# Kernel tuning notes

Measured on AMD Instinct MI355X. Metric: run time of the kernel, lower is better.

## Reference

```python
import jax, jax.numpy as jnp
import numpy as np

IN_DIM, HIDDEN, CLASSES, NBASIS = 1024, 4096, 1000, 16

def setup_inputs() -> dict:
    key = jax.random.key(0)
    ks = jax.random.split(key, 7)
    x = jax.random.normal(ks[0], (4096, IN_DIM), dtype=jnp.float32)
    # FerroelectricBasis params: per-feature tanh basis (centers, scales) + dense mix
    centers = jax.random.normal(ks[1], (IN_DIM, NBASIS), dtype=jnp.float32)
    scales = jax.random.uniform(ks[2], (IN_DIM, NBASIS), dtype=jnp.float32, minval=0.5, maxval=2.0)
    s = 1.0 / np.sqrt(IN_DIM * NBASIS)
    Wb = jax.random.uniform(ks[3], (IN_DIM * NBASIS, HIDDEN), dtype=jnp.float32, minval=-s, maxval=s)
    bb = jax.random.uniform(ks[4], (HIDDEN,), dtype=jnp.float32, minval=-s, maxval=s)
    sh = 1.0 / np.sqrt(HIDDEN)
    Wh = jax.random.uniform(ks[5], (HIDDEN, CLASSES), dtype=jnp.float32, minval=-sh, maxval=sh)
    bh = jax.random.uniform(ks[6], (CLASSES,), dtype=jnp.float32, minval=-sh, maxval=sh)
    return {"x": x, "centers": centers, "scales": scales, "Wb": Wb, "bb": bb, "Wh": Wh, "bh": bh}

def reference(x, centers, scales, Wb, bb, Wh, bh):
    B = x.shape[0]
    # ferroelectric (hysteresis-like) tanh basis expansion: [B, in_dim, num_basis]
    feats = jnp.tanh((x[:, :, None] - centers[None]) * scales[None])
    feats = feats.reshape(B, -1)                      # [B, in_dim*num_basis]
    h = feats @ Wb + bb                               # [B, hidden]
    phi = jax.nn.sigmoid(h)
    logits = phi @ Wh + bh                            # [B, num_classes]
    return logits
```

## Files before the change

### kernel.cpp

```cpp
#include <hip/hip_runtime.h>
#include <hip/hip_bf16.h>

typedef __bf16 bf16x8_t __attribute__((ext_vector_type(8)));
typedef float f32x4_t __attribute__((ext_vector_type(4)));
typedef int i32x4_t __attribute__((ext_vector_type(4)));
typedef int i32x8_t __attribute__((ext_vector_type(8)));

#define GLDS(gp, lp) __builtin_amdgcn_global_load_lds(                        \
    (const __attribute__((address_space(1))) void*)(gp),                      \
    (__attribute__((address_space(3))) void*)(lp), 16, 0, 0)

__device__ __forceinline__ float fast_tanh(float z) {
  float zc = fminf(10.0f, fmaxf(-10.0f, z));
  float e = __expf(2.0f * zc);
  return 1.0f - 2.0f / (e + 1.0f);
}

__device__ __forceinline__ int pack_fp8x4(float a, float b, float c, float d) {
  int w = __builtin_amdgcn_cvt_pk_fp8_f32(a, b, 0, false);
  w = __builtin_amdgcn_cvt_pk_fp8_f32(c, d, w, true);
  return w;
}

__global__ __launch_bounds__(256) void feats_kernel(
    const float* __restrict__ x, const float* __restrict__ c,
    const float* __restrict__ s, unsigned char* __restrict__ out) {
  int idx = blockIdx.x * 256 + threadIdx.x;
  int d = idx & 1023;
  float xv = x[idx];
  const float4* c4 = (const float4*)(c + d * 16);
  const float4* s4 = (const float4*)(s + d * 16);
  int w[4];
#pragma unroll
  for (int g = 0; g < 4; ++g) {
    float4 cc = c4[g], ss = s4[g];
    float t0 = fast_tanh((xv - cc.x) * ss.x);
    float t1 = fast_tanh((xv - cc.y) * ss.y);
    float t2 = fast_tanh((xv - cc.z) * ss.z);
    float t3 = fast_tanh((xv - cc.w) * ss.w);
    w[g] = pack_fp8x4(t0, t1, t2, t3);
  }
  *(uint4*)(out + (size_t)idx * 16) = make_uint4(w[0], w[1], w[2], w[3]);
}

__global__ __launch_bounds__(256) void transpose_fp8(
    const float* __restrict__ src, unsigned char* __restrict__ dst, int R, int C) {
  __shared__ float tile[64][65];
  const int c0 = blockIdx.x * 64, r0 = blockIdx.y * 64;
  const int t = threadIdx.x;
  const int rr = t >> 4, cc4 = (t & 15) * 4;
#pragma unroll
  for (int p = 0; p < 4; ++p) {
    int row = rr + p * 16;
    float4 v = *(const float4*)(src + (size_t)(r0 + row) * C + c0 + cc4);
    tile[row][cc4 + 0] = v.x;
    tile[row][cc4 + 1] = v.y;
    tile[row][cc4 + 2] = v.z;
    tile[row][cc4 + 3] = v.w;
  }
  __syncthreads();
  const int drow = t >> 2, seg = (t & 3) * 16;
  int w[4];
#pragma unroll
  for (int g = 0; g < 4; ++g) {
    float a = tile[seg + g * 4 + 0][drow] * 128.0f;
    float b = tile[seg + g * 4 + 1][drow] * 128.0f;
    float cc = tile[seg + g * 4 + 2][drow] * 128.0f;
    float d = tile[seg + g * 4 + 3][drow] * 128.0f;
    w[g] = pack_fp8x4(a, b, cc, d);
  }
  *(uint4*)(dst + (size_t)(c0 + drow) * R + r0 + seg) = make_uint4(w[0], w[1], w[2], w[3]);
}

__global__ __launch_bounds__(256) void transpose_cast(
    const float* __restrict__ src, __hip_bfloat16* __restrict__ dst,
    int R, int C, int Cpad) {
  __shared__ float tile[64][65];
  const int c0 = blockIdx.x * 64, r0 = blockIdx.y * 64;
  const int t = threadIdx.x;
  const int rr = t >> 4, cc4 = (t & 15) * 4;
#pragma unroll
  for (int p = 0; p < 4; ++p) {
    int row = rr + p * 16;
    int cbase = c0 + cc4;
    float4 v;
    if (cbase + 3 < C) {
      v = *(const float4*)(src + (size_t)(r0 + row) * C + cbase);
    } else {
      v.x = (cbase + 0 < C) ? src[(size_t)(r0 + row) * C + cbase + 0] : 0.0f;
      v.y = (cbase + 1 < C) ? src[(size_t)(r0 + row) * C + cbase + 1] : 0.0f;
      v.z = (cbase + 2 < C) ? src[(size_t)(r0 + row) * C + cbase + 2] : 0.0f;
      v.w = (cbase + 3 < C) ? src[(size_t)(r0 + row) * C + cbase + 3] : 0.0f;
    }
    tile[row][cc4 + 0] = v.x;
    tile[row][cc4 + 1] = v.y;
    tile[row][cc4 + 2] = v.z;
    tile[row][cc4 + 3] = v.w;
  }
  __syncthreads();
#pragma unroll
  for (int p = 0; p < 2; ++p) {
    int i = t + 256 * p;
    int drow = i >> 3;
    int seg = (i & 7) * 8;
    int dc = c0 + drow;
    alignas(16) __hip_bfloat16 vals[8];
#pragma unroll
    for (int j = 0; j < 8; ++j) vals[j] = __float2bfloat16(tile[seg + j][drow]);
    if (dc < Cpad)
      *(uint4*)(dst + (size_t)dc * R + r0 + seg) = *(const uint4*)vals;
  }
}

__global__ __launch_bounds__(512, 2) void gemm1_mx8(
    const unsigned char* __restrict__ A, const unsigned char* __restrict__ Bt,
    const float* __restrict__ bias, __hip_bfloat16* __restrict__ outb,
    int M, int N, int K) {
  __shared__ unsigned char As[2][256 * 128];
  __shared__ unsigned char Bs[2][256 * 128];
  const int tid = threadIdx.x;
  const int wave = tid >> 6, lane = tid & 63;
  const int wm = (wave >> 2) * 128, wn = (wave & 3) * 64;

  const int bid = blockIdx.x;
  const int swz = (bid & 7) * 32 + (bid >> 3);
  const int gq = swz >> 5, u = swz & 31;
  const int gm0 = ((gq >> 1) * 4 + (u >> 3)) * 256;
  const int gn0 = ((gq & 1) * 8 + (u & 7)) * 256;

  const unsigned char* ga[4];
  const unsigned char* gb[4];
  int ldso[4];
#pragma unroll
  for (int p = 0; p < 4; ++p) {
    int c = p * 512 + tid;
    int row = c >> 3;
    int g = (c & 7) ^ (row & 7);
    ga[p] = A + (size_t)(gm0 + row) * K + g * 16;
    gb[p] = Bt + (size_t)(gn0 + row) * K + g * 16;
    ldso[p] = c * 16;
  }

  f32x4_t acc[8][4] = {};
  const int fr = lane & 15, kh = lane >> 4;

#pragma unroll
  for (int p = 0; p < 4; ++p) {
    GLDS(ga[p], &As[0][ldso[p]]);
    GLDS(gb[p], &Bs[0][ldso[p]]);
  }
  __syncthreads();

  const int NT = K >> 7;
  for (int t = 0; t < NT; ++t) {
    const unsigned char* Ac = As[t & 1];
    const unsigned char* Bc = Bs[t & 1];
    unsigned char* An = (unsigned char*)As[(t + 1) & 1];
    unsigned char* Bn = (unsigned char*)Bs[(t + 1) & 1];
    const int k1 = (t + 1) << 7;
    const bool pre = (t + 1 < NT);

    i32x8_t b[4];
#pragma unroll
    for (int j = 0; j < 4; ++j) {
      int rb = wn + j * 16 + fr, sb = rb & 7;
      i32x4_t blo = *(const i32x4_t*)(Bc + rb * 128 + (((2 * kh) ^ sb) * 16));
      i32x4_t bhi = *(const i32x4_t*)(Bc + rb * 128 + (((2 * kh + 1) ^ sb) * 16));
      b[j] = __builtin_shufflevector(blo, bhi, 0, 1, 2, 3, 4, 5, 6, 7);
    }

#pragma unroll
    for (int p = 0; p < 4; ++p) {
      if (pre) {
        GLDS(ga[p] + k1, An + ldso[p]);
        GLDS(gb[p] + k1, Bn + ldso[p]);
      }
      i32x8_t a0, a1;
      {
        int ra = wm + (2 * p + 0) * 16 + fr, sa = ra & 7;
        i32x4_t lo = *(const i32x4_t*)(Ac + ra * 128 + (((2 * kh) ^ sa) * 16));
        i32x4_t hi = *(const i32x4_t*)(Ac + ra * 128 + (((2 * kh + 1) ^ sa) * 16));
        a0 = __builtin_shufflevector(lo, hi, 0, 1, 2, 3, 4, 5, 6, 7);
      }
      {
        int ra = wm + (2 * p + 1) * 16 + fr, sa = ra & 7;
        i32x4_t lo = *(const i32x4_t*)(Ac + ra * 128 + (((2 * kh) ^ sa) * 16));
        i32x4_t hi = *(const i32x4_t*)(Ac + ra * 128 + (((2 * kh + 1) ^ sa) * 16));
        a1 = __builtin_shufflevector(lo, hi, 0, 1, 2, 3, 4, 5, 6, 7);
      }
      __builtin_amdgcn_s_barrier();
      __builtin_amdgcn_s_setprio(1);
#pragma unroll
      for (int j = 0; j < 4; ++j) {
        acc[2 * p + 0][j] = __builtin_amdgcn_mfma_scale_f32_16x16x128_f8f6f4(
            a0, b[j], acc[2 * p + 0][j], 0, 0, 0, 0x7F7F7F7F, 0, 0x7F7F7F7F);
        acc[2 * p + 1][j] = __builtin_amdgcn_mfma_scale_f32_16x16x128_f8f6f4(
            a1, b[j], acc[2 * p + 1][j], 0, 0, 0, 0x7F7F7F7F, 0, 0x7F7F7F7F);
      }
      __builtin_amdgcn_s_setprio(0);
      if (p < 3) __builtin_amdgcn_s_barrier();
    }
    __syncthreads();
  }

  const int cn = lane & 15, cm = (lane >> 4) * 4;
#pragma unroll
  for (int j = 0; j < 4; ++j) {
    int n = gn0 + wn + j * 16 + cn;
    float bv = bias[n];
#pragma unroll
    for (int i = 0; i < 8; ++i) {
#pragma unroll
      for (int r = 0; r < 4; ++r) {
        int m = gm0 + wm + i * 16 + cm + r;
        float v = acc[i][j][r] * 0.0078125f + bv;
        float phi = 1.0f / (1.0f + __expf(-v));
        outb[(size_t)m * N + n] = __float2bfloat16(phi);
      }
    }
  }
}

__global__ __launch_bounds__(256) void gemm2_bt(
    const __hip_bfloat16* __restrict__ A, const __hip_bfloat16* __restrict__ Bt,
    float* __restrict__ outf, int M, int N, int K, int kcount) {
  __shared__ __hip_bfloat16 As[2][128 * 32];
  __shared__ __hip_bfloat16 Bs[2][128 * 32];
  const int tid = threadIdx.x;
  const int wave = tid >> 6, lane = tid & 63;
  const int wm = (wave >> 1) * 64, wn = (wave & 1) * 64;
  const int gm0 = blockIdx.y * 128, gn0 = blockIdx.x * 128;
  const int kbeg = blockIdx.z * kcount;

  const int t1 = tid, t2 = tid + 256;
  const __hip_bfloat16* Ag0 = A + (size_t)(gm0 + (t1 >> 2)) * K + kbeg + (t1 & 3) * 8;
  const __hip_bfloat16* Ag1 = A + (size_t)(gm0 + (t2 >> 2)) * K + kbeg + (t2 & 3) * 8;
  const __hip_bfloat16* Bg0 = Bt + (size_t)(gn0 + (t1 >> 2)) * K + kbeg + (t1 & 3) * 8;
  const __hip_bfloat16* Bg1 = Bt + (size_t)(gn0 + (t2 >> 2)) * K + kbeg + (t2 & 3) * 8;

  f32x4_t acc[4][4] = {};
  const int fr = lane & 15, fk = (lane >> 4) * 8;

  for (int k0 = 0; k0 < kcount; k0 += 64) {
#pragma unroll
    for (int h = 0; h < 2; ++h) {
      GLDS(Ag0 + h * 32, &As[h][t1 * 8]);
      GLDS(Ag1 + h * 32, &As[h][t2 * 8]);
      GLDS(Bg0 + h * 32, &Bs[h][t1 * 8]);
      GLDS(Bg1 + h * 32, &Bs[h][t2 * 8]);
    }
    Ag0 += 64; Ag1 += 64; Bg0 += 64; Bg1 += 64;
    __syncthreads();
#pragma unroll
    for (int h = 0; h < 2; ++h) {
      bf16x8_t a[4], b[4];
#pragma unroll
      for (int i = 0; i < 4; ++i) {
        a[i] = *(const bf16x8_t*)(&As[h][(wm + i * 16 + fr) * 32 + fk]);
        b[i] = *(const bf16x8_t*)(&Bs[h][(wn + i * 16 + fr) * 32 + fk]);
      }
#pragma unroll
      for (int i = 0; i < 4; ++i)
#pragma unroll
        for (int j = 0; j < 4; ++j)
          acc[i][j] = __builtin_amdgcn_mfma_f32_16x16x32_bf16(a[i], b[j], acc[i][j], 0, 0, 0);
    }
    __syncthreads();
  }

  const int cn = lane & 15, cm = (lane >> 4) * 4;
#pragma unroll
  for (int j = 0; j < 4; ++j) {
    int n = gn0 + wn + j * 16 + cn;
#pragma unroll
    for (int i = 0; i < 4; ++i)
#pragma unroll
      for (int r = 0; r < 4; ++r) {
        int m = gm0 + wm + i * 16 + cm + r;
        outf[((size_t)blockIdx.z * M + m) * N + n] = acc[i][j][r];
      }
  }
}

__global__ __launch_bounds__(256) void reduce4_kernel(
    const float* __restrict__ p, const float* __restrict__ bh,
    float* __restrict__ out) {
  int n = blockIdx.x * 256 + threadIdx.x;
  int m = blockIdx.y;
  const size_t zs = (size_t)4096 * 1024;
  if (n < 1000) {
    size_t o = (size_t)m * 1024 + n;
    out[(size_t)m * 1000 + n] = p[o] + p[zs + o] + p[2 * zs + o] + p[3 * zs + o] + bh[n];
  }
}

extern "C" void kernel_launch(void* const* d_in, const int* in_sizes, int n_in,
                              void* d_out, int out_size, void* d_ws, size_t ws_size,
                              hipStream_t stream) {
  const float* x = (const float*)d_in[0];
  const float* centers = (const float*)d_in[1];
  const float* scales = (const float*)d_in[2];
  const float* Wb = (const float*)d_in[3];
  const float* bb = (const float*)d_in[4];
  const float* Wh = (const float*)d_in[5];
  const float* bh = (const float*)d_in[6];
  float* out = (float*)d_out;

  unsigned char* feats = (unsigned char*)d_ws;
  unsigned char* Wbt = feats + (size_t)4096 * 16384;
  __hip_bfloat16* phi = (__hip_bfloat16*)(Wbt + (size_t)4096 * 16384);
  __hip_bfloat16* Wht = phi + (size_t)4096 * 4096;
  float* partial = (float*)d_ws;

  feats_kernel<<<dim3(16384), dim3(256), 0, stream>>>(x, centers, scales, feats);
  transpose_fp8<<<dim3(64, 256), dim3(256), 0, stream>>>(Wb, Wbt, 16384, 4096);
  transpose_cast<<<dim3(16, 64), dim3(256), 0, stream>>>(Wh, Wht, 4096, 1000, 1024);
  gemm1_mx8<<<dim3(256), dim3(512), 0, stream>>>(feats, Wbt, bb, phi, 4096, 4096, 16384);
  gemm2_bt<<<dim3(8, 32, 4), dim3(256), 0, stream>>>(phi, Wht, partial, 4096, 1024, 4096, 1024);
  reduce4_kernel<<<dim3(4, 4096), dim3(256), 0, stream>>>(partial, bh, out);
}
```

Baseline: 773.8 us.

## Drop split-K in second GEMM, double-buffer it, and simplify GEMM1 inner loop

The second GEMM no longer splits K four ways into fp32 partials followed by a reduction kernel. It now computes the full K per block with double-buffered LDS prefetch and writes the bias-added logits directly, removing the partial-buffer traffic and one launch. GEMM1's inner loop now issues all next-tile prefetches up front and runs the MFMA loop without the per-stage barriers. The trade-off is fewer blocks for GEMM2 (256 instead of 1024), which may underfill the GPU, and the GEMM1 change alters how LDS reads and MFMAs interleave across waves.

```diff
diff --git a/kernel.cpp b/kernel.cpp
--- a/kernel.cpp
+++ b/kernel.cpp
@@ -158,7 +158,14 @@
     unsigned char* An = (unsigned char*)As[(t + 1) & 1];
     unsigned char* Bn = (unsigned char*)Bs[(t + 1) & 1];
     const int k1 = (t + 1) << 7;
-    const bool pre = (t + 1 < NT);
+
+    if (t + 1 < NT) {
+#pragma unroll
+      for (int p = 0; p < 4; ++p) {
+        GLDS(ga[p] + k1, An + ldso[p]);
+        GLDS(gb[p] + k1, Bn + ldso[p]);
+      }
+    }
 
     i32x8_t b[4];
 #pragma unroll
@@ -169,37 +176,19 @@
       b[j] = __builtin_shufflevector(blo, bhi, 0, 1, 2, 3, 4, 5, 6, 7);
     }
 
-#pragma unroll
-    for (int p = 0; p < 4; ++p) {
-      if (pre) {
-        GLDS(ga[p] + k1, An + ldso[p]);
-        GLDS(gb[p] + k1, Bn + ldso[p]);
-      }
-      i32x8_t a0, a1;
-      {
-        int ra = wm + (2 * p + 0) * 16 + fr, sa = ra & 7;
-        i32x4_t lo = *(const i32x4_t*)(Ac + ra * 128 + (((2 * kh) ^ sa) * 16));
-        i32x4_t hi = *(const i32x4_t*)(Ac + ra * 128 + (((2 * kh + 1) ^ sa) * 16));
-        a0 = __builtin_shufflevector(lo, hi, 0, 1, 2, 3, 4, 5, 6, 7);
-      }
-      {
-        int ra = wm + (2 * p + 1) * 16 + fr, sa = ra & 7;
-        i32x4_t lo = *(const i32x4_t*)(Ac + ra * 128 + (((2 * kh) ^ sa) * 16));
-        i32x4_t hi = *(const i32x4_t*)(Ac + ra * 128 + (((2 * kh + 1) ^ sa) * 16));
-        a1 = __builtin_shufflevector(lo, hi, 0, 1, 2, 3, 4, 5, 6, 7);
-      }
-      __builtin_amdgcn_s_barrier();
-      __builtin_amdgcn_s_setprio(1);
-#pragma unroll
-      for (int j = 0; j < 4; ++j) {
-        acc[2 * p + 0][j] = __builtin_amdgcn_mfma_scale_f32_16x16x128_f8f6f4(
-            a0, b[j], acc[2 * p + 0][j], 0, 0, 0, 0x7F7F7F7F, 0, 0x7F7F7F7F);
-        acc[2 * p + 1][j] = __builtin_amdgcn_mfma_scale_f32_16x16x128_f8f6f4(
-            a1, b[j], acc[2 * p + 1][j], 0, 0, 0, 0x7F7F7F7F, 0, 0x7F7F7F7F);
-      }
-      __builtin_amdgcn_s_setprio(0);
-      if (p < 3) __builtin_amdgcn_s_barrier();
-    }
+    __builtin_amdgcn_s_setprio(1);
+#pragma unroll
+    for (int i = 0; i < 8; ++i) {
+      int ra = wm + i * 16 + fr, sa = ra & 7;
+      i32x4_t lo = *(const i32x4_t*)(Ac + ra * 128 + (((2 * kh) ^ sa) * 16));
+      i32x4_t hi = *(const i32x4_t*)(Ac + ra * 128 + (((2 * kh + 1) ^ sa) * 16));
+      i32x8_t a = __builtin_shufflevector(lo, hi, 0, 1, 2, 3, 4, 5, 6, 7);
+#pragma unroll
+      for (int j = 0; j < 4; ++j)
+        acc[i][j] = __builtin_amdgcn_mfma_scale_f32_16x16x128_f8f6f4(
+            a, b[j], acc[i][j], 0, 0, 0, 0x7F7F7F7F, 0, 0x7F7F7F7F);
+    }
+    __builtin_amdgcn_s_setprio(0);
     __syncthreads();
   }
 
@@ -221,43 +210,57 @@
   }
 }
 
-__global__ __launch_bounds__(256) void gemm2_bt(
+__global__ __launch_bounds__(256) void gemm2_full(
     const __hip_bfloat16* __restrict__ A, const __hip_bfloat16* __restrict__ Bt,
-    float* __restrict__ outf, int M, int N, int K, int kcount) {
-  __shared__ __hip_bfloat16 As[2][128 * 32];
-  __shared__ __hip_bfloat16 Bs[2][128 * 32];
+    const float* __restrict__ bh, float* __restrict__ out,
+    int M, int N, int K) {
+  __shared__ __hip_bfloat16 As[2][2][128 * 32];
+  __shared__ __hip_bfloat16 Bs[2][2][128 * 32];
   const int tid = threadIdx.x;
   const int wave = tid >> 6, lane = tid & 63;
   const int wm = (wave >> 1) * 64, wn = (wave & 1) * 64;
   const int gm0 = blockIdx.y * 128, gn0 = blockIdx.x * 128;
-  const int kbeg = blockIdx.z * kcount;
 
   const int t1 = tid, t2 = tid + 256;
-  const __hip_bfloat16* Ag0 = A + (size_t)(gm0 + (t1 >> 2)) * K + kbeg + (t1 & 3) * 8;
-  const __hip_bfloat16* Ag1 = A + (size_t)(gm0 + (t2 >> 2)) * K + kbeg + (t2 & 3) * 8;
-  const __hip_bfloat16* Bg0 = Bt + (size_t)(gn0 + (t1 >> 2)) * K + kbeg + (t1 & 3) * 8;
-  const __hip_bfloat16* Bg1 = Bt + (size_t)(gn0 + (t2 >> 2)) * K + kbeg + (t2 & 3) * 8;
+  const __hip_bfloat16* Ag0 = A + (size_t)(gm0 + (t1 >> 2)) * K + (t1 & 3) * 8;
+  const __hip_bfloat16* Ag1 = A + (size_t)(gm0 + (t2 >> 2)) * K + (t2 & 3) * 8;
+  const __hip_bfloat16* Bg0 = Bt + (size_t)(gn0 + (t1 >> 2)) * K + (t1 & 3) * 8;
+  const __hip_bfloat16* Bg1 = Bt + (size_t)(gn0 + (t2 >> 2)) * K + (t2 & 3) * 8;
 
   f32x4_t acc[4][4] = {};
   const int fr = lane & 15, fk = (lane >> 4) * 8;
 
-  for (int k0 = 0; k0 < kcount; k0 += 64) {
-#pragma unroll
-    for (int h = 0; h < 2; ++h) {
-      GLDS(Ag0 + h * 32, &As[h][t1 * 8]);
-      GLDS(Ag1 + h * 32, &As[h][t2 * 8]);
-      GLDS(Bg0 + h * 32, &Bs[h][t1 * 8]);
-      GLDS(Bg1 + h * 32, &Bs[h][t2 * 8]);
-    }
-    Ag0 += 64; Ag1 += 64; Bg0 += 64; Bg1 += 64;
-    __syncthreads();
+#pragma unroll
+  for (int h = 0; h < 2; ++h) {
+    GLDS(Ag0 + h * 32, &As[0][h][t1 * 8]);
+    GLDS(Ag1 + h * 32, &As[0][h][t2 * 8]);
+    GLDS(Bg0 + h * 32, &Bs[0][h][t1 * 8]);
+    GLDS(Bg1 + h * 32, &Bs[0][h][t2 * 8]);
+  }
+  Ag0 += 64; Ag1 += 64; Bg0 += 64; Bg1 += 64;
+  __syncthreads();
+
+  const int nk = K >> 6;
+  for (int it = 0; it < nk; ++it) {
+    const int cur = it & 1;
+    if (it + 1 < nk) {
+      const int nxt = cur ^ 1;
+#pragma unroll
+      for (int h = 0; h < 2; ++h) {
+        GLDS(Ag0 + h * 32, &As[nxt][h][t1 * 8]);
+        GLDS(Ag1 + h * 32, &As[nxt][h][t2 * 8]);
+        GLDS(Bg0 + h * 32, &Bs[nxt][h][t1 * 8]);
+        GLDS(Bg1 + h * 32, &Bs[nxt][h][t2 * 8]);
+      }
+      Ag0 += 64; Ag1 += 64; Bg0 += 64; Bg1 += 64;
+    }
 #pragma unroll
     for (int h = 0; h < 2; ++h) {
       bf16x8_t a[4], b[4];
 #pragma unroll
       for (int i = 0; i < 4; ++i) {
-        a[i] = *(const bf16x8_t*)(&As[h][(wm + i * 16 + fr) * 32 + fk]);
-        b[i] = *(const bf16x8_t*)(&Bs[h][(wn + i * 16 + fr) * 32 + fk]);
+        a[i] = *(const bf16x8_t*)(&As[cur][h][(wm + i * 16 + fr) * 32 + fk]);
+        b[i] = *(const bf16x8_t*)(&Bs[cur][h][(wn + i * 16 + fr) * 32 + fk]);
       }
 #pragma unroll
       for (int i = 0; i < 4; ++i)
@@ -272,25 +275,16 @@
 #pragma unroll
   for (int j = 0; j < 4; ++j) {
     int n = gn0 + wn + j * 16 + cn;
-#pragma unroll
-    for (int i = 0; i < 4; ++i)
-#pragma unroll
-      for (int r = 0; r < 4; ++r) {
-        int m = gm0 + wm + i * 16 + cm + r;
-        outf[((size_t)blockIdx.z * M + m) * N + n] = acc[i][j][r];
-      }
-  }
-}
-
-__global__ __launch_bounds__(256) void reduce4_kernel(
-    const float* __restrict__ p, const float* __restrict__ bh,
-    float* __restrict__ out) {
-  int n = blockIdx.x * 256 + threadIdx.x;
-  int m = blockIdx.y;
-  const size_t zs = (size_t)4096 * 1024;
-  if (n < 1000) {
-    size_t o = (size_t)m * 1024 + n;
-    out[(size_t)m * 1000 + n] = p[o] + p[zs + o] + p[2 * zs + o] + p[3 * zs + o] + bh[n];
+    if (n < 1000) {
+      float bv = bh[n];
+#pragma unroll
+      for (int i = 0; i < 4; ++i)
+#pragma unroll
+        for (int r = 0; r < 4; ++r) {
+          int m = gm0 + wm + i * 16 + cm + r;
+          out[(size_t)m * 1000 + n] = acc[i][j][r] + bv;
+        }
+    }
   }
 }
 
@@ -310,12 +304,10 @@
   unsigned char* Wbt = feats + (size_t)4096 * 16384;
   __hip_bfloat16* phi = (__hip_bfloat16*)(Wbt + (size_t)4096 * 16384);
   __hip_bfloat16* Wht = phi + (size_t)4096 * 4096;
-  float* partial = (float*)d_ws;
 
   feats_kernel<<<dim3(16384), dim3(256), 0, stream>>>(x, centers, scales, feats);
   transpose_fp8<<<dim3(64, 256), dim3(256), 0, stream>>>(Wb, Wbt, 16384, 4096);
   transpose_cast<<<dim3(16, 64), dim3(256), 0, stream>>>(Wh, Wht, 4096, 1000, 1024);
   gemm1_mx8<<<dim3(256), dim3(512), 0, stream>>>(feats, Wbt, bb, phi, 4096, 4096, 16384);
-  gemm2_bt<<<dim3(8, 32, 4), dim3(256), 0, stream>>>(phi, Wht, partial, 4096, 1024, 4096, 1024);
-  reduce4_kernel<<<dim3(4, 4096), dim3(256), 0, stream>>>(partial, bh, out);
-}
+  gemm2_full<<<dim3(8, 32), dim3(256), 0, stream>>>(phi, Wht, bh, out, 4096, 1024, 4096);
+}
```

Result: slower. 837.4 us (+8.2%).
